# Optimization experiments

Measured on AMD Instinct MI355X. Metric: run time of the kernel, lower is better.

Reference implementation:

```python
import jax, jax.numpy as jnp
import numpy as np

HID, H, KV, S, B = 2048, 32, 8, 2048, 2
D = HID // H           # head_dim = 64
G = H // KV            # query heads per kv head = 4


def setup_inputs() -> dict:
    key = jax.random.key(0)
    ks = jax.random.split(key, 10)
    sc = 0.02
    kv_dim = HID * KV // H  # 512
    return {
        "x": jax.random.normal(ks[0], (B, S, HID), jnp.float32),
        "attention_mask": jnp.zeros((B, S), jnp.float32),
        "Wq": jax.random.normal(ks[1], (HID, HID), jnp.float32) * sc,
        "bq": jnp.zeros((HID,), jnp.float32),
        "Wk": jax.random.normal(ks[2], (kv_dim, HID), jnp.float32) * sc,
        "bk": jnp.zeros((kv_dim,), jnp.float32),
        "Wv": jax.random.normal(ks[3], (kv_dim, HID), jnp.float32) * sc,
        "bv": jnp.zeros((kv_dim,), jnp.float32),
        "Wo": jax.random.normal(ks[4], (HID, HID), jnp.float32) * sc,
        "bo": jnp.zeros((HID,), jnp.float32),
    }


def reference(x, attention_mask, Wq, bq, Wk, bk, Wv, bv, Wo, bo):
    Bx, Sx, _ = x.shape
    # projections (torch Linear: x @ W.T + b)
    q = x @ Wq.T + bq                                  # [B,S,HID]
    k = x @ Wk.T + bk                                  # [B,S,KV*D]
    v = x @ Wv.T + bv
    # split heads: [B,S,H,D] -> [B,H,S,D]; then group q: [B,KV,G,S,D]
    q = q.reshape(Bx, Sx, H, D).transpose(0, 2, 1, 3).reshape(Bx, KV, G, Sx, D)
    k = k.reshape(Bx, Sx, KV, D).transpose(0, 2, 1, 3)  # [B,KV,S,D]
    v = v.reshape(Bx, Sx, KV, D).transpose(0, 2, 1, 3)
    scale = 1.0 / jnp.sqrt(jnp.float32(D))
    scores = jnp.einsum('bkgsd,bktd->bkgst', q, k) * scale  # [B,KV,G,S,S]
    scores = scores + attention_mask[:, None, None, None, :]
    attn = jax.nn.softmax(scores, axis=-1)
    out = jnp.einsum('bkgst,bktd->bkgsd', attn, v)          # [B,KV,G,S,D]
    out = out.reshape(Bx, H, Sx, D).transpose(0, 2, 1, 3).reshape(Bx, Sx, HID)
    return out @ Wo.T + bo
```

## Files before the change

### kernel.cpp

```cpp
#include <hip/hip_runtime.h>
#include <hip/hip_bf16.h>
#include <stdint.h>

typedef __hip_bfloat16 bf16;
typedef __attribute__((ext_vector_type(8))) short bf16x8;
typedef __attribute__((ext_vector_type(4))) float f32x4;
typedef __attribute__((ext_vector_type(16))) float f32x16;
typedef __attribute__((ext_vector_type(4))) int i32x4;
typedef __attribute__((ext_vector_type(2))) int i32x2;

#define B_   2
#define S_   2048
#define HID_ 2048
#define H_   32
#define KV_  8
#define D_   64
#define KVD_ (KV_ * D_)
#define NT_  (S_ / 64)
#define LOG2E 1.4426950408889634f

__device__ __forceinline__ void gload_lds16(const void* g, void* l) {
  __builtin_amdgcn_global_load_lds(
      (const __attribute__((address_space(1))) uint32_t*)g,
      (__attribute__((address_space(3))) uint32_t*)l, 16, 0, 0);
}
__device__ __forceinline__ float fexp2(float x) { return __builtin_amdgcn_exp2f(x); }

__device__ __forceinline__ uint32_t cvtpk_bf16(float lo, float hi) {
  uint32_t r;
  asm("v_cvt_pk_bf16_f32 %0, %1, %2" : "=v"(r) : "v"(lo), "v"(hi));
  return r;
}
__device__ __forceinline__ void plane32_swap(uint32_t& a, uint32_t& b) {
  i32x2 r = __builtin_amdgcn_permlane32_swap((int)a, (int)b, false, false);
  a = (uint32_t)r[0]; b = (uint32_t)r[1];
}

struct CvtJob { const float* s; bf16* d; int n4; };
__global__ __launch_bounds__(256) void cvt_multi(
    CvtJob j0, CvtJob j1, CvtJob j2, CvtJob j3, CvtJob j4) {
  CvtJob j;
  switch (blockIdx.y) {
    case 0: j = j0; break;
    case 1: j = j1; break;
    case 2: j = j2; break;
    case 3: j = j3; break;
    default: j = j4; break;
  }
  int i = blockIdx.x * blockDim.x + threadIdx.x;
  const int stride = gridDim.x * blockDim.x;
  for (; i < j.n4; i += stride) {
    float4 v = ((const float4*)j.s)[i];
    bf16 t[4];
    t[0] = __float2bfloat16(v.x);
    t[1] = __float2bfloat16(v.y);
    t[2] = __float2bfloat16(v.z);
    t[3] = __float2bfloat16(v.w);
    *reinterpret_cast<uint64_t*>(j.d + 4 * (size_t)i) = *reinterpret_cast<uint64_t*>(t);
  }
}

__global__ __launch_bounds__(256) void mask_prep(
    const float* __restrict__ m, float* __restrict__ o, int n) {
  int i = blockIdx.x * blockDim.x + threadIdx.x;
  if (i < n) o[i] = m[i] * LOG2E;
}

__global__ __launch_bounds__(256, 3) void gemm_qkv(
    const bf16* __restrict__ A,
    const bf16* __restrict__ Wqp, const bf16* __restrict__ Wkp, const bf16* __restrict__ Wvp,
    const float* __restrict__ bqp, const float* __restrict__ bkp, const float* __restrict__ bvp,
    bf16* __restrict__ Cq, bf16* __restrict__ Ck, bf16* __restrict__ Cv) {
  const int lid0 = blockIdx.y * gridDim.x + blockIdx.x;
  const int q8 = (int)(gridDim.x * gridDim.y) >> 3;
  const int lid = (lid0 & 7) * q8 + (lid0 >> 3);
  const int bm = lid & 31;
  const int bn_all = lid >> 5;

  const bf16* W; const float* bias; int bn;
  if (bn_all < 16)      { W = Wqp; bias = bqp; bn = bn_all; }
  else if (bn_all < 20) { W = Wkp; bias = bkp; bn = bn_all - 16; }
  else                  { W = Wvp; bias = bvp; bn = bn_all - 20; }
  const float oscale = (bn_all < 16) ? (0.125f * LOG2E) : 1.0f;

  __shared__ __align__(16) bf16 As[128 * 64];
  __shared__ __align__(16) bf16 Bs[128 * 64];
  const int tid = threadIdx.x;
  const int lane = tid & 63, wid = tid >> 6;
  const int wr = wid >> 1, wc = wid & 1;
  const int K = HID_;

  f32x4 acc[4][4] = {};

  for (int k0 = 0; k0 < K; k0 += 64) {
    __syncthreads();
#pragma unroll
    for (int c = 0; c < 4; ++c) {
      const int r = c * 32 + wid * 8 + (lane >> 3);
      const int gcolb = ((lane & 7) * 16) ^ ((r & 7) << 4);
      gload_lds16(A + (size_t)(bm * 128 + r) * K + k0 + (gcolb >> 1),
                  &As[(c * 32 + wid * 8) * 64]);
      gload_lds16(W + (size_t)(bn * 128 + r) * K + k0 + (gcolb >> 1),
                  &Bs[(c * 32 + wid * 8) * 64]);
    }
    __syncthreads();
#pragma unroll
    for (int ks = 0; ks < 2; ++ks) {
      bf16x8 af[4], bfr[4];
#pragma unroll
      for (int i = 0; i < 4; ++i) {
        const int ra = wr * 64 + i * 16 + (lane & 15);
        const int ka = (ks * 64 + ((lane >> 4) << 4)) ^ ((ra & 7) << 4);
        af[i] = *(const bf16x8*)((const char*)As + ra * 128 + ka);
        const int rb = wc * 64 + i * 16 + (lane & 15);
        const int kb = (ks * 64 + ((lane >> 4) << 4)) ^ ((rb & 7) << 4);
        bfr[i] = *(const bf16x8*)((const char*)Bs + rb * 128 + kb);
      }
      __builtin_amdgcn_s_setprio(1);
#pragma unroll
      for (int i = 0; i < 4; ++i)
#pragma unroll
        for (int j = 0; j < 4; ++j)
          acc[i][j] = __builtin_amdgcn_mfma_f32_16x16x32_bf16(af[i], bfr[j], acc[i][j], 0, 0, 0);
      __builtin_amdgcn_s_setprio(0);
    }
  }

  if (bn_all < 16) {
#pragma unroll
    for (int j = 0; j < 4; ++j) {
      const int n = bn * 128 + wc * 64 + j * 16 + (lane & 15);
      const float bv = bias[n];
#pragma unroll
      for (int i = 0; i < 4; ++i) {
        const int mb = bm * 128 + wr * 64 + i * 16 + ((lane >> 4) << 2);
#pragma unroll
        for (int e = 0; e < 4; ++e)
          Cq[(size_t)(mb + e) * HID_ + n] = __float2bfloat16((acc[i][j][e] + bv) * oscale);
      }
    }
  } else if (bn_all < 20) {
#pragma unroll
    for (int j = 0; j < 4; ++j) {
      const int n = bn * 128 + wc * 64 + j * 16 + (lane & 15);
      const float bv = bias[n];
#pragma unroll
      for (int i = 0; i < 4; ++i) {
        const int mb = bm * 128 + wr * 64 + i * 16 + ((lane >> 4) << 2);
#pragma unroll
        for (int e = 0; e < 4; ++e)
          Ck[(size_t)(mb + e) * KVD_ + n] = __float2bfloat16(acc[i][j][e] + bv);
      }
    }
  } else {
#pragma unroll
    for (int j = 0; j < 4; ++j) {
      const int n = bn * 128 + wc * 64 + j * 16 + (lane & 15);
      const int kvh = n >> 6, d = n & 63;
      const float bv = bias[n];
#pragma unroll
      for (int i = 0; i < 4; ++i) {
        const int m0 = bm * 128 + wr * 64 + i * 16 + ((lane >> 4) << 2);
        const int b = m0 >> 11, s0 = m0 & (S_ - 1);
        bf16 t4[4];
#pragma unroll
        for (int e = 0; e < 4; ++e) t4[e] = __float2bfloat16(acc[i][j][e] + bv);
        *reinterpret_cast<uint64_t*>(
            Cv + (((size_t)b * KV_ + kvh) * D_ + d) * S_ + s0) =
            *reinterpret_cast<uint64_t*>(t4);
      }
    }
  }
}

__global__ __launch_bounds__(256, 2) void gemm_out(
    const bf16* __restrict__ A, const bf16* __restrict__ W,
    const float* __restrict__ bias, float* __restrict__ C) {
  const int lid0 = blockIdx.y * gridDim.x + blockIdx.x;
  const int q8 = (int)(gridDim.x * gridDim.y) >> 3;
  const int lid = (lid0 & 7) * q8 + (lid0 >> 3);
  const int bm = lid & 31;
  const int bn = lid >> 5;

  __shared__ __align__(16) bf16 As[128 * 64];
  __shared__ __align__(16) bf16 Bs[128 * 64];
  const int tid = threadIdx.x;
  const int lane = tid & 63, wid = tid >> 6;
  const int wr = wid >> 1, wc = wid & 1;
  const int K = HID_, N = HID_;

  f32x4 acc[4][4] = {};

  for (int k0 = 0; k0 < K; k0 += 64) {
    __syncthreads();
#pragma unroll
    for (int c = 0; c < 4; ++c) {
      const int r = c * 32 + wid * 8 + (lane >> 3);
      const int gcolb = ((lane & 7) * 16) ^ ((r & 7) << 4);
      gload_lds16(A + (size_t)(bm * 128 + r) * K + k0 + (gcolb >> 1),
                  &As[(c * 32 + wid * 8) * 64]);
      gload_lds16(W + (size_t)(bn * 128 + r) * K + k0 + (gcolb >> 1),
                  &Bs[(c * 32 + wid * 8) * 64]);
    }
    __syncthreads();
#pragma unroll
    for (int ks = 0; ks < 2; ++ks) {
      bf16x8 af[4], bfr[4];
#pragma unroll
      for (int i = 0; i < 4; ++i) {
        const int ra = wr * 64 + i * 16 + (lane & 15);
        const int ka = (ks * 64 + ((lane >> 4) << 4)) ^ ((ra & 7) << 4);
        af[i] = *(const bf16x8*)((const char*)As + ra * 128 + ka);
        const int rb = wc * 64 + i * 16 + (lane & 15);
        const int kb = (ks * 64 + ((lane >> 4) << 4)) ^ ((rb & 7) << 4);
        bfr[i] = *(const bf16x8*)((const char*)Bs + rb * 128 + kb);
      }
      __builtin_amdgcn_s_setprio(1);
#pragma unroll
      for (int i = 0; i < 4; ++i)
#pragma unroll
        for (int j = 0; j < 4; ++j)
          acc[i][j] = __builtin_amdgcn_mfma_f32_16x16x32_bf16(af[i], bfr[j], acc[i][j], 0, 0, 0);
      __builtin_amdgcn_s_setprio(0);
    }
  }

#pragma unroll
  for (int j = 0; j < 4; ++j) {
    const int n = bn * 128 + wc * 64 + j * 16 + (lane & 15);
    const float bv = bias[n];
#pragma unroll
    for (int i = 0; i < 4; ++i) {
      const int mb = bm * 128 + wr * 64 + i * 16 + ((lane >> 4) << 2);
#pragma unroll
      for (int e = 0; e < 4; ++e) {
        C[(size_t)(mb + e) * N + n] = acc[i][j][e] + bv;
      }
    }
  }
}

__global__ __launch_bounds__(256, 2) void attn_fwd(
    const bf16* __restrict__ qb, const bf16* __restrict__ kb,
    const bf16* __restrict__ vtb, const float* __restrict__ maskL,
    bf16* __restrict__ ob) {
  const int lid0 = blockIdx.y * gridDim.x + blockIdx.x;
  const int q8 = (int)(gridDim.x * gridDim.y) >> 3;
  const int lid = (lid0 & 7) * q8 + (lid0 >> 3);
  const int qtile = lid & 7;
  const int headid = lid >> 3;
  const int b = headid >> 5, h = headid & (H_ - 1);
  const int kv = h >> 2;
  const int tid = threadIdx.x, lane = tid & 63, wid = tid >> 6;
  const int l31 = lane & 31, hi = lane >> 5;

  __shared__ __align__(16) bf16 Ks[2][64 * 64];
  __shared__ __align__(16) bf16 VTs[2][64 * 64];

  const bf16* qh = qb + (size_t)b * S_ * HID_ + h * 64;
  const bf16* kh = kb + (size_t)b * S_ * KVD_ + kv * 64;
  const bf16* vth = vtb + (size_t)(b * KV_ + kv) * D_ * S_;
  const float* mrow = maskL + (size_t)b * S_;

  const int qrowbase = qtile * 256 + wid * 64;
  bf16x8 qf[2][4];
#pragma unroll
  for (int qs = 0; qs < 2; ++qs)
#pragma unroll
    for (int ks = 0; ks < 4; ++ks)
      qf[qs][ks] = *(const bf16x8*)(qh + (size_t)(qrowbase + qs * 32 + l31) * HID_ + ks * 16 + hi * 8);

  bf16x8 ones;
#pragma unroll
  for (int i = 0; i < 8; ++i) ones[i] = (short)0x3F80;

  f32x16 o0[2] = {}, o1[2] = {};
  f32x16 lacc0 = {}, lacc1 = {};

#pragma unroll
  for (int c = 0; c < 2; ++c) {
    const int r = c * 32 + wid * 8 + (lane >> 3);
    const int gcolb = ((lane & 7) * 16) ^ ((r & 7) << 4);
    gload_lds16(kh + (size_t)r * KVD_ + (gcolb >> 1), &Ks[0][(c * 32 + wid * 8) * 64]);
    gload_lds16(vth + (size_t)r * S_ + (gcolb >> 1), &VTs[0][(c * 32 + wid * 8) * 64]);
  }
  __syncthreads();

  for (int t = 0; t < NT_; ++t) {
    const int cur = t & 1, nxt = cur ^ 1;

    if (t < NT_ - 1) {
#pragma unroll
      for (int c = 0; c < 2; ++c) {
        const int r = c * 32 + wid * 8 + (lane >> 3);
        const int gcolb = ((lane & 7) * 16) ^ ((r & 7) << 4);
        gload_lds16(kh + (size_t)((t + 1) * 64 + r) * KVD_ + (gcolb >> 1),
                    &Ks[nxt][(c * 32 + wid * 8) * 64]);
        gload_lds16(vth + (size_t)r * S_ + (t + 1) * 64 + (gcolb >> 1),
                    &VTs[nxt][(c * 32 + wid * 8) * 64]);
      }
    }

    f32x16 s0[2], s1[2];
#pragma unroll
    for (int kbv = 0; kbv < 2; ++kbv) {
#pragma unroll
      for (int rq = 0; rq < 4; ++rq) {
        const f32x4 m4 = *(const f32x4*)(mrow + t * 64 + kbv * 32 + rq * 8 + 4 * hi);
#pragma unroll
        for (int e = 0; e < 4; ++e) {
          s0[kbv][rq * 4 + e] = m4[e];
          s1[kbv][rq * 4 + e] = m4[e];
        }
      }
    }

    bf16x8 kf0[4], kf1[4];
#pragma unroll
    for (int ks = 0; ks < 4; ++ks) {
      const int rk = l31;
      const int kbyte = (ks * 32 + hi * 16) ^ ((rk & 7) << 4);
      kf0[ks] = *(const bf16x8*)((const char*)&Ks[cur][0] + rk * 128 + kbyte);
    }
    __builtin_amdgcn_s_setprio(1);
#pragma unroll
    for (int ks = 0; ks < 4; ++ks)
      s0[0] = __builtin_amdgcn_mfma_f32_32x32x16_bf16(kf0[ks], qf[0][ks], s0[0], 0, 0, 0);
#pragma unroll
    for (int ks = 0; ks < 4; ++ks)
      s1[0] = __builtin_amdgcn_mfma_f32_32x32x16_bf16(kf0[ks], qf[1][ks], s1[0], 0, 0, 0);
    __builtin_amdgcn_s_setprio(0);
#pragma unroll
    for (int ks = 0; ks < 4; ++ks) {
      const int rk = 32 + l31;
      const int kbyte = (ks * 32 + hi * 16) ^ ((rk & 7) << 4);
      kf1[ks] = *(const bf16x8*)((const char*)&Ks[cur][0] + rk * 128 + kbyte);
    }
    __builtin_amdgcn_s_setprio(1);
#pragma unroll
    for (int ks = 0; ks < 4; ++ks)
      s0[1] = __builtin_amdgcn_mfma_f32_32x32x16_bf16(kf1[ks], qf[0][ks], s0[1], 0, 0, 0);
    __builtin_amdgcn_s_setprio(0);

    bf16x8 pa0[2][2], pa1[2][2];
#pragma unroll
    for (int r = 0; r < 16; ++r) s0[0][r] = fexp2(s0[0][r]);
    {
      uint32_t a0 = cvtpk_bf16(s0[0][0], s0[0][1]);
      uint32_t b0 = cvtpk_bf16(s0[0][4], s0[0][5]);
      plane32_swap(a0, b0);
      uint32_t a1 = cvtpk_bf16(s0[0][2], s0[0][3]);
      uint32_t b1 = cvtpk_bf16(s0[0][6], s0[0][7]);
      plane32_swap(a1, b1);
      i32x4 t0; t0[0] = (int)a0; t0[1] = (int)a1; t0[2] = (int)b0; t0[3] = (int)b1;
      pa0[0][0] = __builtin_bit_cast(bf16x8, t0);
      uint32_t a2 = cvtpk_bf16(s0[0][8], s0[0][9]);
      uint32_t b2 = cvtpk_bf16(s0[0][12], s0[0][13]);
      plane32_swap(a2, b2);
      uint32_t a3 = cvtpk_bf16(s0[0][10], s0[0][11]);
      uint32_t b3 = cvtpk_bf16(s0[0][14], s0[0][15]);
      plane32_swap(a3, b3);
      i32x4 t1; t1[0] = (int)a2; t1[1] = (int)a3; t1[2] = (int)b2; t1[3] = (int)b3;
      pa0[0][1] = __builtin_bit_cast(bf16x8, t1);
    }

    __builtin_amdgcn_s_setprio(1);
#pragma unroll
    for (int ks = 0; ks < 4; ++ks)
      s1[1] = __builtin_amdgcn_mfma_f32_32x32x16_bf16(kf1[ks], qf[1][ks], s1[1], 0, 0, 0);
    __builtin_amdgcn_s_setprio(0);

#pragma unroll
    for (int r = 0; r < 16; ++r) s0[1][r] = fexp2(s0[1][r]);
    {
      uint32_t a0 = cvtpk_bf16(s0[1][0], s0[1][1]);
      uint32_t b0 = cvtpk_bf16(s0[1][4], s0[1][5]);
      plane32_swap(a0, b0);
      uint32_t a1 = cvtpk_bf16(s0[1][2], s0[1][3]);
      uint32_t b1 = cvtpk_bf16(s0[1][6], s0[1][7]);
      plane32_swap(a1, b1);
      i32x4 t0; t0[0] = (int)a0; t0[1] = (int)a1; t0[2] = (int)b0; t0[3] = (int)b1;
      pa0[1][0] = __builtin_bit_cast(bf16x8, t0);
      uint32_t a2 = cvtpk_bf16(s0[1][8], s0[1][9]);
      uint32_t b2 = cvtpk_bf16(s0[1][12], s0[1][13]);
      plane32_swap(a2, b2);
      uint32_t a3 = cvtpk_bf16(s0[1][10], s0[1][11]);
      uint32_t b3 = cvtpk_bf16(s0[1][14], s0[1][15]);
      plane32_swap(a3, b3);
      i32x4 t1; t1[0] = (int)a2; t1[1] = (int)a3; t1[2] = (int)b2; t1[3] = (int)b3;
      pa0[1][1] = __builtin_bit_cast(bf16x8, t1);
    }

    bf16x8 vf[2][4];
#pragma unroll
    for (int db = 0; db < 2; ++db)
#pragma unroll
      for (int kk = 0; kk < 4; ++kk) {
        const int kbv = kk >> 1, ks2 = kk & 1;
        const int rd = db * 32 + l31;
        const int vbyte = (kbv * 64 + ks2 * 32 + hi * 16) ^ ((rd & 7) << 4);
        vf[db][kk] = *(const bf16x8*)((const char*)&VTs[cur][0] + rd * 128 + vbyte);
      }

    __builtin_amdgcn_s_setprio(1);
#pragma unroll
    for (int kk = 0; kk < 4; ++kk)
      lacc0 = __builtin_amdgcn_mfma_f32_32x32x16_bf16(pa0[kk >> 1][kk & 1], ones, lacc0, 0, 0, 0);
#pragma unroll
    for (int db = 0; db < 2; ++db)
#pragma unroll
      for (int kk = 0; kk < 4; ++kk)
        o0[db] = __builtin_amdgcn_mfma_f32_32x32x16_bf16(pa0[kk >> 1][kk & 1], vf[db][kk], o0[db], 0, 0, 0);
    __builtin_amdgcn_s_setprio(0);

#pragma unroll
    for (int kbv = 0; kbv < 2; ++kbv) {
#pragma unroll
      for (int r = 0; r < 16; ++r) s1[kbv][r] = fexp2(s1[kbv][r]);
      uint32_t a0 = cvtpk_bf16(s1[kbv][0], s1[kbv][1]);
      uint32_t b0 = cvtpk_bf16(s1[kbv][4], s1[kbv][5]);
      plane32_swap(a0, b0);
      uint32_t a1 = cvtpk_bf16(s1[kbv][2], s1[kbv][3]);
      uint32_t b1 = cvtpk_bf16(s1[kbv][6], s1[kbv][7]);
      plane32_swap(a1, b1);
      i32x4 t0; t0[0] = (int)a0; t0[1] = (int)a1; t0[2] = (int)b0; t0[3] = (int)b1;
      pa1[kbv][0] = __builtin_bit_cast(bf16x8, t0);
      uint32_t a2 = cvtpk_bf16(s1[kbv][8], s1[kbv][9]);
      uint32_t b2 = cvtpk_bf16(s1[kbv][12], s1[kbv][13]);
      plane32_swap(a2, b2);
      uint32_t a3 = cvtpk_bf16(s1[kbv][10], s1[kbv][11]);
      uint32_t b3 = cvtpk_bf16(s1[kbv][14], s1[kbv][15]);
      plane32_swap(a3, b3);
      i32x4 t1; t1[0] = (int)a2; t1[1] = (int)a3; t1[2] = (int)b2; t1[3] = (int)b3;
      pa1[kbv][1] = __builtin_bit_cast(bf16x8, t1);
    }

    __builtin_amdgcn_s_setprio(1);
#pragma unroll
    for (int kk = 0; kk < 4; ++kk)
      lacc1 = __builtin_amdgcn_mfma_f32_32x32x16_bf16(pa1[kk >> 1][kk & 1], ones, lacc1, 0, 0, 0);
#pragma unroll
    for (int db = 0; db < 2; ++db)
#pragma unroll
      for (int kk = 0; kk < 4; ++kk)
        o1[db] = __builtin_amdgcn_mfma_f32_32x32x16_bf16(pa1[kk >> 1][kk & 1], vf[db][kk], o1[db], 0, 0, 0);
    __builtin_amdgcn_s_setprio(0);

    __syncthreads();
  }

#pragma unroll
  for (int r = 0; r < 16; ++r) {
    const int q_out = (r & 3) + 8 * (r >> 2) + 4 * hi;
    {
      const float inv = 1.0f / lacc0[r];
      const int srow = qrowbase + q_out;
      ob[((size_t)b * S_ + srow) * HID_ + h * 64 + l31] = __float2bfloat16(o0[0][r] * inv);
      ob[((size_t)b * S_ + srow) * HID_ + h * 64 + 32 + l31] = __float2bfloat16(o0[1][r] * inv);
    }
    {
      const float inv = 1.0f / lacc1[r];
      const int srow = qrowbase + 32 + q_out;
      ob[((size_t)b * S_ + srow) * HID_ + h * 64 + l31] = __float2bfloat16(o1[0][r] * inv);
      ob[((size_t)b * S_ + srow) * HID_ + h * 64 + 32 + l31] = __float2bfloat16(o1[1][r] * inv);
    }
  }
}

extern "C" void kernel_launch(void* const* d_in, const int* in_sizes, int n_in,
                              void* d_out, int out_size, void* d_ws, size_t ws_size,
                              hipStream_t stream) {
  (void)in_sizes; (void)n_in; (void)out_size; (void)ws_size;
  const float* x  = (const float*)d_in[0];
  const float* am = (const float*)d_in[1];
  const float* Wq = (const float*)d_in[2];
  const float* bq = (const float*)d_in[3];
  const float* Wk = (const float*)d_in[4];
  const float* bk = (const float*)d_in[5];
  const float* Wv = (const float*)d_in[6];
  const float* bv = (const float*)d_in[7];
  const float* Wo = (const float*)d_in[8];
  const float* bo = (const float*)d_in[9];
  float* out = (float*)d_out;

  const size_t XE  = (size_t)B_ * S_ * HID_;
  const size_t WQE = (size_t)HID_ * HID_;
  const size_t WKE = (size_t)KVD_ * HID_;
  const size_t QE  = (size_t)B_ * S_ * HID_;
  const size_t KE  = (size_t)B_ * S_ * KVD_;

  bf16* xb  = (bf16*)d_ws;
  bf16* wqb = xb + XE;
  bf16* wkb = wqb + WQE;
  bf16* wvb = wkb + WKE;
  bf16* wob = wvb + WKE;
  bf16* qbuf = wob + WQE;
  bf16* kbuf = qbuf + QE;
  bf16* vtbuf = kbuf + KE;
  bf16* abuf = vtbuf + KE;
  float* maskL = (float*)(abuf + XE);

  dim3 blk(256);
  CvtJob jx  = { x,  xb,  (int)(XE / 4) };
  CvtJob jwq = { Wq, wqb, (int)(WQE / 4) };
  CvtJob jwk = { Wk, wkb, (int)(WKE / 4) };
  CvtJob jwv = { Wv, wvb, (int)(WKE / 4) };
  CvtJob jwo = { Wo, wob, (int)(WQE / 4) };
  cvt_multi<<<dim3(512, 5), blk, 0, stream>>>(jx, jwq, jwk, jwv, jwo);
  mask_prep<<<(B_ * S_ + 255) / 256, blk, 0, stream>>>(am, maskL, B_ * S_);

  const int M = B_ * S_;
  gemm_qkv<<<dim3(M / 128, 24), blk, 0, stream>>>(xb, wqb, wkb, wvb, bq, bk, bv,
                                                  qbuf, kbuf, vtbuf);
  attn_fwd<<<dim3(S_ / 256, B_ * H_), blk, 0, stream>>>(qbuf, kbuf, vtbuf, maskL, abuf);
  gemm_out<<<dim3(M / 128, HID_ / 128), blk, 0, stream>>>(abuf, wob, bo, out);
}
```

Before: 190.5 us.

## Stage 128-key K/V tiles per barrier and fold mask scaling into attention

The attention loop now stages 128 keys of K and V^T per double-buffered LDS tile and processes them as two 64-key sub-blocks, halving the number of barriers and prefetch rounds. The V^T tile uses a 256-byte row stride with a 16-way XOR swizzle. The separate mask_prep launch is removed, and the mask is multiplied by log2(e) inside the attention kernel instead. The trade-off is doubled LDS use (64 KB per block), which may limit occupancy against the two blocks requested by the launch bounds.

```diff
diff --git a/kernel.cpp b/kernel.cpp
--- a/kernel.cpp
+++ b/kernel.cpp
@@ -16,7 +16,7 @@
 #define KV_  8
 #define D_   64
 #define KVD_ (KV_ * D_)
-#define NT_  (S_ / 64)
+#define NT2_ (S_ / 128)
 #define LOG2E 1.4426950408889634f
 
 __device__ __forceinline__ void gload_lds16(const void* g, void* l) {
@@ -60,12 +60,6 @@
   }
 }
 
-__global__ __launch_bounds__(256) void mask_prep(
-    const float* __restrict__ m, float* __restrict__ o, int n) {
-  int i = blockIdx.x * blockDim.x + threadIdx.x;
-  if (i < n) o[i] = m[i] * LOG2E;
-}
-
 __global__ __launch_bounds__(256, 3) void gemm_qkv(
     const bf16* __restrict__ A,
     const bf16* __restrict__ Wqp, const bf16* __restrict__ Wkp, const bf16* __restrict__ Wvp,
@@ -242,7 +236,7 @@
 
 __global__ __launch_bounds__(256, 2) void attn_fwd(
     const bf16* __restrict__ qb, const bf16* __restrict__ kb,
-    const bf16* __restrict__ vtb, const float* __restrict__ maskL,
+    const bf16* __restrict__ vtb, const float* __restrict__ mask,
     bf16* __restrict__ ob) {
   const int lid0 = blockIdx.y * gridDim.x + blockIdx.x;
   const int q8 = (int)(gridDim.x * gridDim.y) >> 3;
@@ -254,13 +248,13 @@
   const int tid = threadIdx.x, lane = tid & 63, wid = tid >> 6;
   const int l31 = lane & 31, hi = lane >> 5;
 
-  __shared__ __align__(16) bf16 Ks[2][64 * 64];
-  __shared__ __align__(16) bf16 VTs[2][64 * 64];
+  __shared__ __align__(16) bf16 Ks[2][128 * 64];
+  __shared__ __align__(16) bf16 VTs[2][64 * 128];
 
   const bf16* qh = qb + (size_t)b * S_ * HID_ + h * 64;
   const bf16* kh = kb + (size_t)b * S_ * KVD_ + kv * 64;
   const bf16* vth = vtb + (size_t)(b * KV_ + kv) * D_ * S_;
-  const float* mrow = maskL + (size_t)b * S_;
+  const float* mrow = mask + (size_t)b * S_;
 
   const int qrowbase = qtile * 256 + wid * 64;
   bf16x8 qf[2][4];
@@ -277,174 +271,179 @@
   f32x16 o0[2] = {}, o1[2] = {};
   f32x16 lacc0 = {}, lacc1 = {};
 
-#pragma unroll
-  for (int c = 0; c < 2; ++c) {
-    const int r = c * 32 + wid * 8 + (lane >> 3);
-    const int gcolb = ((lane & 7) * 16) ^ ((r & 7) << 4);
-    gload_lds16(kh + (size_t)r * KVD_ + (gcolb >> 1), &Ks[0][(c * 32 + wid * 8) * 64]);
-    gload_lds16(vth + (size_t)r * S_ + (gcolb >> 1), &VTs[0][(c * 32 + wid * 8) * 64]);
-  }
+#define STAGE_TILE(buf, t2)                                                        \
+  {                                                                                \
+    _Pragma("unroll")                                                              \
+    for (int c = 0; c < 4; ++c) {                                                  \
+      const int r = c * 32 + wid * 8 + (lane >> 3);                                \
+      const int gcolb = ((lane & 7) * 16) ^ ((r & 7) << 4);                        \
+      gload_lds16(kh + (size_t)((t2) * 128 + r) * KVD_ + (gcolb >> 1),             \
+                  &Ks[buf][(c * 32 + wid * 8) * 64]);                              \
+    }                                                                              \
+    _Pragma("unroll")                                                              \
+    for (int c = 0; c < 4; ++c) {                                                  \
+      const int rv = c * 16 + wid * 4 + (lane >> 4);                               \
+      const int gv = ((lane & 15) * 16) ^ ((rv & 15) << 4);                        \
+      gload_lds16(vth + (size_t)rv * S_ + (t2) * 128 + (gv >> 1),                  \
+                  &VTs[buf][(c * 16 + wid * 4) * 128]);                            \
+    }                                                                              \
+  }
+
+  STAGE_TILE(0, 0);
   __syncthreads();
 
-  for (int t = 0; t < NT_; ++t) {
+  for (int t = 0; t < NT2_; ++t) {
     const int cur = t & 1, nxt = cur ^ 1;
-
-    if (t < NT_ - 1) {
-#pragma unroll
-      for (int c = 0; c < 2; ++c) {
-        const int r = c * 32 + wid * 8 + (lane >> 3);
-        const int gcolb = ((lane & 7) * 16) ^ ((r & 7) << 4);
-        gload_lds16(kh + (size_t)((t + 1) * 64 + r) * KVD_ + (gcolb >> 1),
-                    &Ks[nxt][(c * 32 + wid * 8) * 64]);
-        gload_lds16(vth + (size_t)r * S_ + (t + 1) * 64 + (gcolb >> 1),
-                    &VTs[nxt][(c * 32 + wid * 8) * 64]);
-      }
-    }
-
-    f32x16 s0[2], s1[2];
-#pragma unroll
-    for (int kbv = 0; kbv < 2; ++kbv) {
-#pragma unroll
-      for (int rq = 0; rq < 4; ++rq) {
-        const f32x4 m4 = *(const f32x4*)(mrow + t * 64 + kbv * 32 + rq * 8 + 4 * hi);
-#pragma unroll
-        for (int e = 0; e < 4; ++e) {
-          s0[kbv][rq * 4 + e] = m4[e];
-          s1[kbv][rq * 4 + e] = m4[e];
+    if (t < NT2_ - 1) STAGE_TILE(nxt, t + 1);
+
+#pragma unroll
+    for (int sub = 0; sub < 2; ++sub) {
+      f32x16 s0[2], s1[2];
+#pragma unroll
+      for (int kbv = 0; kbv < 2; ++kbv) {
+#pragma unroll
+        for (int rq = 0; rq < 4; ++rq) {
+          const f32x4 m4 = *(const f32x4*)(mrow + t * 128 + sub * 64 + kbv * 32 + rq * 8 + 4 * hi);
+#pragma unroll
+          for (int e = 0; e < 4; ++e) {
+            const float mv = m4[e] * LOG2E;
+            s0[kbv][rq * 4 + e] = mv;
+            s1[kbv][rq * 4 + e] = mv;
+          }
         }
       }
-    }
-
-    bf16x8 kf0[4], kf1[4];
-#pragma unroll
-    for (int ks = 0; ks < 4; ++ks) {
-      const int rk = l31;
-      const int kbyte = (ks * 32 + hi * 16) ^ ((rk & 7) << 4);
-      kf0[ks] = *(const bf16x8*)((const char*)&Ks[cur][0] + rk * 128 + kbyte);
-    }
-    __builtin_amdgcn_s_setprio(1);
-#pragma unroll
-    for (int ks = 0; ks < 4; ++ks)
-      s0[0] = __builtin_amdgcn_mfma_f32_32x32x16_bf16(kf0[ks], qf[0][ks], s0[0], 0, 0, 0);
-#pragma unroll
-    for (int ks = 0; ks < 4; ++ks)
-      s1[0] = __builtin_amdgcn_mfma_f32_32x32x16_bf16(kf0[ks], qf[1][ks], s1[0], 0, 0, 0);
-    __builtin_amdgcn_s_setprio(0);
-#pragma unroll
-    for (int ks = 0; ks < 4; ++ks) {
-      const int rk = 32 + l31;
-      const int kbyte = (ks * 32 + hi * 16) ^ ((rk & 7) << 4);
-      kf1[ks] = *(const bf16x8*)((const char*)&Ks[cur][0] + rk * 128 + kbyte);
-    }
-    __builtin_amdgcn_s_setprio(1);
-#pragma unroll
-    for (int ks = 0; ks < 4; ++ks)
-      s0[1] = __builtin_amdgcn_mfma_f32_32x32x16_bf16(kf1[ks], qf[0][ks], s0[1], 0, 0, 0);
-    __builtin_amdgcn_s_setprio(0);
-
-    bf16x8 pa0[2][2], pa1[2][2];
-#pragma unroll
-    for (int r = 0; r < 16; ++r) s0[0][r] = fexp2(s0[0][r]);
-    {
-      uint32_t a0 = cvtpk_bf16(s0[0][0], s0[0][1]);
-      uint32_t b0 = cvtpk_bf16(s0[0][4], s0[0][5]);
-      plane32_swap(a0, b0);
-      uint32_t a1 = cvtpk_bf16(s0[0][2], s0[0][3]);
-      uint32_t b1 = cvtpk_bf16(s0[0][6], s0[0][7]);
-      plane32_swap(a1, b1);
-      i32x4 t0; t0[0] = (int)a0; t0[1] = (int)a1; t0[2] = (int)b0; t0[3] = (int)b1;
-      pa0[0][0] = __builtin_bit_cast(bf16x8, t0);
-      uint32_t a2 = cvtpk_bf16(s0[0][8], s0[0][9]);
-      uint32_t b2 = cvtpk_bf16(s0[0][12], s0[0][13]);
-      plane32_swap(a2, b2);
-      uint32_t a3 = cvtpk_bf16(s0[0][10], s0[0][11]);
-      uint32_t b3 = cvtpk_bf16(s0[0][14], s0[0][15]);
-      plane32_swap(a3, b3);
-      i32x4 t1; t1[0] = (int)a2; t1[1] = (int)a3; t1[2] = (int)b2; t1[3] = (int)b3;
-      pa0[0][1] = __builtin_bit_cast(bf16x8, t1);
-    }
-
-    __builtin_amdgcn_s_setprio(1);
-#pragma unroll
-    for (int ks = 0; ks < 4; ++ks)
-      s1[1] = __builtin_amdgcn_mfma_f32_32x32x16_bf16(kf1[ks], qf[1][ks], s1[1], 0, 0, 0);
-    __builtin_amdgcn_s_setprio(0);
-
-#pragma unroll
-    for (int r = 0; r < 16; ++r) s0[1][r] = fexp2(s0[1][r]);
-    {
-      uint32_t a0 = cvtpk_bf16(s0[1][0], s0[1][1]);
-      uint32_t b0 = cvtpk_bf16(s0[1][4], s0[1][5]);
-      plane32_swap(a0, b0);
-      uint32_t a1 = cvtpk_bf16(s0[1][2], s0[1][3]);
-      uint32_t b1 = cvtpk_bf16(s0[1][6], s0[1][7]);
-      plane32_swap(a1, b1);
-      i32x4 t0; t0[0] = (int)a0; t0[1] = (int)a1; t0[2] = (int)b0; t0[3] = (int)b1;
-      pa0[1][0] = __builtin_bit_cast(bf16x8, t0);
-      uint32_t a2 = cvtpk_bf16(s0[1][8], s0[1][9]);
-      uint32_t b2 = cvtpk_bf16(s0[1][12], s0[1][13]);
-      plane32_swap(a2, b2);
-      uint32_t a3 = cvtpk_bf16(s0[1][10], s0[1][11]);
-      uint32_t b3 = cvtpk_bf16(s0[1][14], s0[1][15]);
-      plane32_swap(a3, b3);
-      i32x4 t1; t1[0] = (int)a2; t1[1] = (int)a3; t1[2] = (int)b2; t1[3] = (int)b3;
-      pa0[1][1] = __builtin_bit_cast(bf16x8, t1);
-    }
-
-    bf16x8 vf[2][4];
-#pragma unroll
-    for (int db = 0; db < 2; ++db)
-#pragma unroll
-      for (int kk = 0; kk < 4; ++kk) {
-        const int kbv = kk >> 1, ks2 = kk & 1;
-        const int rd = db * 32 + l31;
-        const int vbyte = (kbv * 64 + ks2 * 32 + hi * 16) ^ ((rd & 7) << 4);
-        vf[db][kk] = *(const bf16x8*)((const char*)&VTs[cur][0] + rd * 128 + vbyte);
-      }
-
-    __builtin_amdgcn_s_setprio(1);
-#pragma unroll
-    for (int kk = 0; kk < 4; ++kk)
-      lacc0 = __builtin_amdgcn_mfma_f32_32x32x16_bf16(pa0[kk >> 1][kk & 1], ones, lacc0, 0, 0, 0);
-#pragma unroll
-    for (int db = 0; db < 2; ++db)
+
+      bf16x8 kf0[4], kf1[4];
+#pragma unroll
+      for (int ks = 0; ks < 4; ++ks) {
+        const int rk = sub * 64 + l31;
+        const int kbyte = (ks * 32 + hi * 16) ^ ((rk & 7) << 4);
+        kf0[ks] = *(const bf16x8*)((const char*)&Ks[cur][0] + rk * 128 + kbyte);
+      }
+      __builtin_amdgcn_s_setprio(1);
+#pragma unroll
+      for (int ks = 0; ks < 4; ++ks)
+        s0[0] = __builtin_amdgcn_mfma_f32_32x32x16_bf16(kf0[ks], qf[0][ks], s0[0], 0, 0, 0);
+#pragma unroll
+      for (int ks = 0; ks < 4; ++ks)
+        s1[0] = __builtin_amdgcn_mfma_f32_32x32x16_bf16(kf0[ks], qf[1][ks], s1[0], 0, 0, 0);
+      __builtin_amdgcn_s_setprio(0);
+#pragma unroll
+      for (int ks = 0; ks < 4; ++ks) {
+        const int rk = sub * 64 + 32 + l31;
+        const int kbyte = (ks * 32 + hi * 16) ^ ((rk & 7) << 4);
+        kf1[ks] = *(const bf16x8*)((const char*)&Ks[cur][0] + rk * 128 + kbyte);
+      }
+      __builtin_amdgcn_s_setprio(1);
+#pragma unroll
+      for (int ks = 0; ks < 4; ++ks)
+        s0[1] = __builtin_amdgcn_mfma_f32_32x32x16_bf16(kf1[ks], qf[0][ks], s0[1], 0, 0, 0);
+      __builtin_amdgcn_s_setprio(0);
+
+      bf16x8 pa0[2][2], pa1[2][2];
+#pragma unroll
+      for (int r = 0; r < 16; ++r) s0[0][r] = fexp2(s0[0][r]);
+      {
+        uint32_t a0 = cvtpk_bf16(s0[0][0], s0[0][1]);
+        uint32_t b0 = cvtpk_bf16(s0[0][4], s0[0][5]);
+        plane32_swap(a0, b0);
+        uint32_t a1 = cvtpk_bf16(s0[0][2], s0[0][3]);
+        uint32_t b1 = cvtpk_bf16(s0[0][6], s0[0][7]);
+        plane32_swap(a1, b1);
+        i32x4 t0; t0[0] = (int)a0; t0[1] = (int)a1; t0[2] = (int)b0; t0[3] = (int)b1;
+        pa0[0][0] = __builtin_bit_cast(bf16x8, t0);
+        uint32_t a2 = cvtpk_bf16(s0[0][8], s0[0][9]);
+        uint32_t b2 = cvtpk_bf16(s0[0][12], s0[0][13]);
+        plane32_swap(a2, b2);
+        uint32_t a3 = cvtpk_bf16(s0[0][10], s0[0][11]);
+        uint32_t b3 = cvtpk_bf16(s0[0][14], s0[0][15]);
+        plane32_swap(a3, b3);
+        i32x4 t1; t1[0] = (int)a2; t1[1] = (int)a3; t1[2] = (int)b2; t1[3] = (int)b3;
+        pa0[0][1] = __builtin_bit_cast(bf16x8, t1);
+      }
+
+      __builtin_amdgcn_s_setprio(1);
+#pragma unroll
+      for (int ks = 0; ks < 4; ++ks)
+        s1[1] = __builtin_amdgcn_mfma_f32_32x32x16_bf16(kf1[ks], qf[1][ks], s1[1], 0, 0, 0);
+      __builtin_amdgcn_s_setprio(0);
+
+#pragma unroll
+      for (int r = 0; r < 16; ++r) s0[1][r] = fexp2(s0[1][r]);
+      {
+        uint32_t a0 = cvtpk_bf16(s0[1][0], s0[1][1]);
+        uint32_t b0 = cvtpk_bf16(s0[1][4], s0[1][5]);
+        plane32_swap(a0, b0);
+        uint32_t a1 = cvtpk_bf16(s0[1][2], s0[1][3]);
+        uint32_t b1 = cvtpk_bf16(s0[1][6], s0[1][7]);
+        plane32_swap(a1, b1);
+        i32x4 t0; t0[0] = (int)a0; t0[1] = (int)a1; t0[2] = (int)b0; t0[3] = (int)b1;
+        pa0[1][0] = __builtin_bit_cast(bf16x8, t0);
+        uint32_t a2 = cvtpk_bf16(s0[1][8], s0[1][9]);
+        uint32_t b2 = cvtpk_bf16(s0[1][12], s0[1][13]);
+        plane32_swap(a2, b2);
+        uint32_t a3 = cvtpk_bf16(s0[1][10], s0[1][11]);
+        uint32_t b3 = cvtpk_bf16(s0[1][14], s0[1][15]);
+        plane32_swap(a3, b3);
+        i32x4 t1; t1[0] = (int)a2; t1[1] = (int)a3; t1[2] = (int)b2; t1[3] = (int)b3;
+        pa0[1][1] = __builtin_bit_cast(bf16x8, t1);
+      }
+
+      bf16x8 vf[2][4];
+#pragma unroll
+      for (int db = 0; db < 2; ++db)
+#pragma unroll
+        for (int kk = 0; kk < 4; ++kk) {
+          const int kbv = kk >> 1, ks2 = kk & 1;
+          const int rd = db * 32 + l31;
+          const int vbyte = (sub * 128 + kbv * 64 + ks2 * 32 + hi * 16) ^ ((rd & 15) << 4);
+          vf[db][kk] = *(const bf16x8*)((const char*)&VTs[cur][0] + rd * 256 + vbyte);
+        }
+
+      __builtin_amdgcn_s_setprio(1);
 #pragma unroll
       for (int kk = 0; kk < 4; ++kk)
-        o0[db] = __builtin_amdgcn_mfma_f32_32x32x16_bf16(pa0[kk >> 1][kk & 1], vf[db][kk], o0[db], 0, 0, 0);
-    __builtin_amdgcn_s_setprio(0);
-
-#pragma unroll
-    for (int kbv = 0; kbv < 2; ++kbv) {
-#pragma unroll
-      for (int r = 0; r < 16; ++r) s1[kbv][r] = fexp2(s1[kbv][r]);
-      uint32_t a0 = cvtpk_bf16(s1[kbv][0], s1[kbv][1]);
-      uint32_t b0 = cvtpk_bf16(s1[kbv][4], s1[kbv][5]);
-      plane32_swap(a0, b0);
-      uint32_t a1 = cvtpk_bf16(s1[kbv][2], s1[kbv][3]);
-      uint32_t b1 = cvtpk_bf16(s1[kbv][6], s1[kbv][7]);
-      plane32_swap(a1, b1);
-      i32x4 t0; t0[0] = (int)a0; t0[1] = (int)a1; t0[2] = (int)b0; t0[3] = (int)b1;
-      pa1[kbv][0] = __builtin_bit_cast(bf16x8, t0);
-      uint32_t a2 = cvtpk_bf16(s1[kbv][8], s1[kbv][9]);
-      uint32_t b2 = cvtpk_bf16(s1[kbv][12], s1[kbv][13]);
-      plane32_swap(a2, b2);
-      uint32_t a3 = cvtpk_bf16(s1[kbv][10], s1[kbv][11]);
-      uint32_t b3 = cvtpk_bf16(s1[kbv][14], s1[kbv][15]);
-      plane32_swap(a3, b3);
-      i32x4 t1; t1[0] = (int)a2; t1[1] = (int)a3; t1[2] = (int)b2; t1[3] = (int)b3;
-      pa1[kbv][1] = __builtin_bit_cast(bf16x8, t1);
-    }
-
-    __builtin_amdgcn_s_setprio(1);
-#pragma unroll
-    for (int kk = 0; kk < 4; ++kk)
-      lacc1 = __builtin_amdgcn_mfma_f32_32x32x16_bf16(pa1[kk >> 1][kk & 1], ones, lacc1, 0, 0, 0);
-#pragma unroll
-    for (int db = 0; db < 2; ++db)
+        lacc0 = __builtin_amdgcn_mfma_f32_32x32x16_bf16(pa0[kk >> 1][kk & 1], ones, lacc0, 0, 0, 0);
+#pragma unroll
+      for (int db = 0; db < 2; ++db)
+#pragma unroll
+        for (int kk = 0; kk < 4; ++kk)
+          o0[db] = __builtin_amdgcn_mfma_f32_32x32x16_bf16(pa0[kk >> 1][kk & 1], vf[db][kk], o0[db], 0, 0, 0);
+      __builtin_amdgcn_s_setprio(0);
+
+#pragma unroll
+      for (int kbv = 0; kbv < 2; ++kbv) {
+#pragma unroll
+        for (int r = 0; r < 16; ++r) s1[kbv][r] = fexp2(s1[kbv][r]);
+        uint32_t a0 = cvtpk_bf16(s1[kbv][0], s1[kbv][1]);
+        uint32_t b0 = cvtpk_bf16(s1[kbv][4], s1[kbv][5]);
+        plane32_swap(a0, b0);
+        uint32_t a1 = cvtpk_bf16(s1[kbv][2], s1[kbv][3]);
+        uint32_t b1 = cvtpk_bf16(s1[kbv][6], s1[kbv][7]);
+        plane32_swap(a1, b1);
+        i32x4 t0; t0[0] = (int)a0; t0[1] = (int)a1; t0[2] = (int)b0; t0[3] = (int)b1;
+        pa1[kbv][0] = __builtin_bit_cast(bf16x8, t0);
+        uint32_t a2 = cvtpk_bf16(s1[kbv][8], s1[kbv][9]);
+        uint32_t b2 = cvtpk_bf16(s1[kbv][12], s1[kbv][13]);
+        plane32_swap(a2, b2);
+        uint32_t a3 = cvtpk_bf16(s1[kbv][10], s1[kbv][11]);
+        uint32_t b3 = cvtpk_bf16(s1[kbv][14], s1[kbv][15]);
+        plane32_swap(a3, b3);
+        i32x4 t1; t1[0] = (int)a2; t1[1] = (int)a3; t1[2] = (int)b2; t1[3] = (int)b3;
+        pa1[kbv][1] = __builtin_bit_cast(bf16x8, t1);
+      }
+
+      __builtin_amdgcn_s_setprio(1);
 #pragma unroll
       for (int kk = 0; kk < 4; ++kk)
-        o1[db] = __builtin_amdgcn_mfma_f32_32x32x16_bf16(pa1[kk >> 1][kk & 1], vf[db][kk], o1[db], 0, 0, 0);
-    __builtin_amdgcn_s_setprio(0);
+        lacc1 = __builtin_amdgcn_mfma_f32_32x32x16_bf16(pa1[kk >> 1][kk & 1], ones, lacc1, 0, 0, 0);
+#pragma unroll
+      for (int db = 0; db < 2; ++db)
+#pragma unroll
+        for (int kk = 0; kk < 4; ++kk)
+          o1[db] = __builtin_amdgcn_mfma_f32_32x32x16_bf16(pa1[kk >> 1][kk & 1], vf[db][kk], o1[db], 0, 0, 0);
+      __builtin_amdgcn_s_setprio(0);
+    }
 
     __syncthreads();
   }
@@ -465,6 +464,7 @@
       ob[((size_t)b * S_ + srow) * HID_ + h * 64 + 32 + l31] = __float2bfloat16(o1[1][r] * inv);
     }
   }
+#undef STAGE_TILE
 }
 
 extern "C" void kernel_launch(void* const* d_in, const int* in_sizes, int n_in,
@@ -498,7 +498,6 @@
   bf16* kbuf = qbuf + QE;
   bf16* vtbuf = kbuf + KE;
   bf16* abuf = vtbuf + KE;
-  float* maskL = (float*)(abuf + XE);
 
   dim3 blk(256);
   CvtJob jx  = { x,  xb,  (int)(XE / 4) };
@@ -507,11 +506,10 @@
   CvtJob jwv = { Wv, wvb, (int)(WKE / 4) };
   CvtJob jwo = { Wo, wob, (int)(WQE / 4) };
   cvt_multi<<<dim3(512, 5), blk, 0, stream>>>(jx, jwq, jwk, jwv, jwo);
-  mask_prep<<<(B_ * S_ + 255) / 256, blk, 0, stream>>>(am, maskL, B_ * S_);
 
   const int M = B_ * S_;
   gemm_qkv<<<dim3(M / 128, 24), blk, 0, stream>>>(xb, wqb, wkb, wvb, bq, bk, bv,
                                                   qbuf, kbuf, vtbuf);
-  attn_fwd<<<dim3(S_ / 256, B_ * H_), blk, 0, stream>>>(qbuf, kbuf, vtbuf, maskL, abuf);
+  attn_fwd<<<dim3(S_ / 256, B_ * H_), blk, 0, stream>>>(qbuf, kbuf, vtbuf, am, abuf);
   gemm_out<<<dim3(M / 128, HID_ / 128), blk, 0, stream>>>(abuf, wob, bo, out);
 }
```

After: 190.6 us. Within noise of the previous version (+0.1%).
